# Kernel optimization log

Measured on AMD Instinct MI355X. Metric: run time of the kernel, lower is better.

Reference implementation:

```python
import jax, jax.numpy as jnp
import numpy as np

B, N, FEA = 64, 512, 102      # batch, motif points, feature cols (1 weight + 100 dist + 1 atom idx)
E = 10                         # expansion_size
d = 256                        # embed_dim
H = 4                          # num_heads
D = d * H                      # encoder working dim (embed_dim*num_heads)
L = 3                          # n_encoders
NATOM = 100                    # atom_init table rows
NDIST = FEA - 2                # 100 distance columns


def _ln(x, g, b, eps=1e-5):
    m = jnp.mean(x, -1, keepdims=True)
    v = jnp.mean((x - m) ** 2, -1, keepdims=True)
    return (x - m) / jnp.sqrt(v + eps) * g + b


def setup_inputs() -> dict:
    key = jax.random.key(0)
    ks = iter(jax.random.split(key, 40))

    def p(shape):
        return 0.02 * jax.random.normal(next(ks), shape, dtype=jnp.float32)

    # features: [:,:,0] = PDD weights (positive, row-normalized), [:,:,1:-1] = distances, [:,:,-1] = atom idx
    w = jax.random.uniform(next(ks), (B, N, 1), dtype=jnp.float32) + 1e-3
    w = w / jnp.sum(w, axis=1, keepdims=True)
    dist = jax.random.uniform(next(ks), (B, N, NDIST), dtype=jnp.float32)
    idx = jax.random.randint(next(ks), (B, N, 1), 0, NATOM).astype(jnp.float32)
    features = jnp.concatenate([w, dist, idx], axis=-1)

    inp = {
        "features": features,
        "atom_fea": p((NATOM, 92)),
        "comp_W": p((92, d)), "comp_b": p((d,)),
        "emb_W": p((NDIST * E, d)), "emb_b": p((d,)),
        "ln_g": jnp.ones((d,), jnp.float32), "ln_b": jnp.zeros((d,), jnp.float32),
        "enc_emb_W": p((L, d, D)), "enc_emb_b": p((L, D)),
        "enc_Wq_W": p((L, D, D)), "enc_Wq_b": p((L, D)),
        "enc_Wk_W": p((L, D, D)), "enc_Wk_b": p((L, D)),
        "enc_Wv_W": p((L, D, D)), "enc_Wv_b": p((L, D)),
        "enc_inq_W": p((L, D, D)), "enc_inq_b": p((L, D)),   # MHA in_proj (q part)
        "enc_ink_W": p((L, D, D)), "enc_ink_b": p((L, D)),   # MHA in_proj (k part)
        "enc_ln_g": jnp.ones((L, D), jnp.float32), "enc_ln_b": jnp.zeros((L, D), jnp.float32),
        "enc_out_W": p((L, D, d)), "enc_out_b": p((L, d)),
        "out_W": p((d, 1)), "out_b": p((1,)),
    }
    return inp


def reference(features, atom_fea, comp_W, comp_b, emb_W, emb_b, ln_g, ln_b,
              enc_emb_W, enc_emb_b, enc_Wq_W, enc_Wq_b, enc_Wk_W, enc_Wk_b,
              enc_Wv_W, enc_Wv_b, enc_inq_W, enc_inq_b, enc_ink_W, enc_ink_b,
              enc_ln_g, enc_ln_b, enc_out_W, enc_out_b, out_W, out_b):
    w = features[:, :, 0:1]                      # [B,N,1] PDD weights
    feat = features[:, :, 1:]
    idx = feat[:, :, -1].astype(jnp.int32)       # atom type index
    comp = atom_fea[idx] @ comp_W + comp_b       # [B,N,d]
    dist = feat[:, :, :-1]                       # [B,N,NDIST]
    starter = jnp.arange(E, dtype=features.dtype) / E
    de = (1.0 - (dist[..., None] - starter)) ** 2            # [B,N,NDIST,E]
    de = de.reshape(dist.shape[0], dist.shape[1], NDIST * E)
    strf = de @ emb_W + emb_b                    # [B,N,d]
    x = _ln(comp + strf, ln_g, ln_b)
    x_init = x
    dh = D // H
    scale = 1.0 / jnp.sqrt(jnp.asarray(dh, features.dtype))
    for l in range(L):
        e = x @ enc_emb_W[l] + enc_emb_b[l]                  # [B,N,D]
        mask = jnp.sum(jnp.abs(e), -1) == 0.0                # key padding mask [B,N]
        q = (e @ enc_Wq_W[l] + enc_Wq_b[l]) @ enc_inq_W[l] + enc_inq_b[l]
        k = (e @ enc_Wk_W[l] + enc_Wk_b[l]) @ enc_ink_W[l] + enc_ink_b[l]
        qh = q.reshape(q.shape[0], q.shape[1], H, dh)
        kh = k.reshape(k.shape[0], k.shape[1], H, dh)
        scores = jnp.einsum('bqhd,bkhd->bhqk', qh, kh) * scale
        scores = jnp.where(mask[:, None, None, :], -1e9, scores)
        A = jax.nn.softmax(scores, axis=-1).mean(axis=1)     # head-averaged attn weights [B,N,N]
        A = A * jnp.swapaxes(w, -2, -1)                      # external PDD reweighting
        A = A / jnp.sum(A, -1, keepdims=True)
        v = e @ enc_Wv_W[l] + enc_Wv_b[l]
        att = jnp.einsum('bij,bjd->bid', A, v)
        xe = _ln(e + jax.nn.softplus(att), enc_ln_g[l], enc_ln_b[l])
        x = xe @ enc_out_W[l] + enc_out_b[l]                 # back to [B,N,d]
    pooled = jnp.sum(w * (x + x_init), axis=1)               # weighted-sum pool [B,d]
    pooled = _ln(pooled, ln_g, ln_b)
    return pooled @ out_W + out_b                            # [B,1]
```

## Files before the change

kernel.cpp:

```cpp
#include <hip/hip_runtime.h>
#include <hip/hip_bf16.h>

#define PB 64
#define PN 512
#define PFEA 102
#define PE 10
#define PDD 256
#define PH 4
#define PDBIG 1024
#define PL 3
#define PNDIST 100

typedef __attribute__((ext_vector_type(8))) short s8b;
typedef __attribute__((ext_vector_type(4))) float f4;

typedef __attribute__((address_space(1))) const void gvoid_t;
typedef __attribute__((address_space(3))) void lvoid_t;
#define GLDS16(g, s) __builtin_amdgcn_global_load_lds((gvoid_t*)(g), (lvoid_t*)(s), 16, 0, 0)

union bfu { __hip_bfloat16 b; unsigned short u; };

__device__ __forceinline__ float b2f(unsigned short u) {
    return __uint_as_float((unsigned int)u << 16);
}
__device__ __forceinline__ unsigned short f2bu(float v) {
    bfu c; c.b = __float2bfloat16(v); return c.u;
}
__device__ __forceinline__ void split_bf16(float v, __hip_bfloat16& hi, __hip_bfloat16& lo) {
    hi = __float2bfloat16(v);
    lo = __float2bfloat16(v - __bfloat162float(hi));
}
__device__ __forceinline__ void split_u(float v, unsigned short& hu, unsigned short& lu) {
    __hip_bfloat16 h, l; split_bf16(v, h, l);
    bfu c; c.b = h; hu = c.u; c.b = l; lu = c.u;
}

__device__ __forceinline__ float block_sum1(float v, float* red, int tid) {
    #pragma unroll
    for (int off = 32; off >= 1; off >>= 1) v += __shfl_xor(v, off);
    __syncthreads();
    if ((tid & 63) == 0) red[tid >> 6] = v;
    __syncthreads();
    return red[0] + red[1] + red[2] + red[3];
}

template<int NR, bool MAXOP>
__device__ __forceinline__ void block_redN(float* v, float* red, int tid) {
    #pragma unroll
    for (int off = 32; off >= 1; off >>= 1) {
        #pragma unroll
        for (int r = 0; r < NR; ++r) {
            float o = __shfl_xor(v[r], off);
            v[r] = MAXOP ? fmaxf(v[r], o) : (v[r] + o);
        }
    }
    __syncthreads();
    if ((tid & 63) == 0) {
        #pragma unroll
        for (int r = 0; r < NR; ++r) red[(tid >> 6) * NR + r] = v[r];
    }
    __syncthreads();
    #pragma unroll
    for (int r = 0; r < NR; ++r) {
        float a = red[r], b = red[NR + r], c = red[2 * NR + r], d = red[3 * NR + r];
        v[r] = MAXOP ? fmaxf(fmaxf(a, b), fmaxf(c, d)) : ((a + b) + (c + d));
    }
    __syncthreads();
}

__global__ __launch_bounds__(256) void pst_atomproj(
    const float* __restrict__ atom_fea, const float* __restrict__ comp_W,
    float* __restrict__ atomP)
{
    int a = blockIdx.x, tid = threadIdx.x;
    __shared__ float af[92];
    if (tid < 92) af[tid] = atom_fea[a * 92 + tid];
    __syncthreads();
    float s = 0.0f;
    #pragma unroll 4
    for (int k = 0; k < 92; ++k) s = fmaf(af[k], comp_W[k * PDD + tid], s);
    atomP[a * PDD + tid] = s;
}

__global__ __launch_bounds__(256) void pst_embW_reduce(
    const float* __restrict__ emb_W, float* __restrict__ S0, float* __restrict__ S1)
{
    int f = blockIdx.x, tid = threadIdx.x;
    float s0 = 0.0f, s1 = 0.0f;
    #pragma unroll
    for (int t = 0; t < PE; ++t) {
        float w = emb_W[(f * PE + t) * PDD + tid];
        float tf = (float)t / (float)PE;
        s0 += w;
        s1 = fmaf(2.0f * tf, w, s1);
    }
    S0[f * PDD + tid] = s0;
    S1[f * PDD + tid] = s1;
}

__global__ __launch_bounds__(256) void pst_embW_const(
    const float* __restrict__ emb_W, const float* __restrict__ comp_b,
    const float* __restrict__ emb_b, float* __restrict__ Cv)
{
    int tid = threadIdx.x;
    float s = comp_b[tid] + emb_b[tid];
    for (int m = 0; m < PNDIST * PE; ++m) {
        float tf = (float)(m % PE) / (float)PE;
        s = fmaf(tf * tf, emb_W[m * PDD + tid], s);
    }
    Cv[tid] = s;
}

__global__ __launch_bounds__(256) void pst_wext(
    const float* __restrict__ features, float* __restrict__ wvec)
{
    long i = (long)blockIdx.x * 256 + threadIdx.x;
    wvec[i] = features[i * PFEA];
}

__global__ __launch_bounds__(256) void pst_embed16(
    const float* __restrict__ features, const float* __restrict__ atomP,
    const float* __restrict__ S0, const float* __restrict__ S1,
    const float* __restrict__ Cv, const float* __restrict__ ln_g,
    const float* __restrict__ ln_b, unsigned short* __restrict__ xpk)
{
    int r0 = blockIdx.x * 16, tid = threadIdx.x;
    __shared__ float uv[16][PNDIST];
    __shared__ int idxs[16];
    __shared__ float red[64];
    for (int m = tid; m < 16 * PNDIST; m += 256) {
        int r = m / PNDIST, f = m - r * PNDIST;
        uv[r][f] = 1.0f - features[(long)(r0 + r) * PFEA + 1 + f];
    }
    if (tid < 16) idxs[tid] = (int)features[(long)(r0 + tid) * PFEA + PFEA - 1];
    __syncthreads();

    float acc[16];
    float cv = Cv[tid];
    #pragma unroll
    for (int r = 0; r < 16; ++r) acc[r] = cv + atomP[idxs[r] * PDD + tid];
    for (int f = 0; f < PNDIST; f += 4) {
        float s0v[4], s1v[4];
        #pragma unroll
        for (int u = 0; u < 4; ++u) {
            s0v[u] = S0[(f + u) * PDD + tid];
            s1v[u] = S1[(f + u) * PDD + tid];
        }
        #pragma unroll
        for (int u = 0; u < 4; ++u) {
            #pragma unroll
            for (int r = 0; r < 16; ++r) {
                float uu = uv[r][f + u];
                acc[r] = fmaf(uu, fmaf(uu, s0v[u], s1v[u]), acc[r]);
            }
        }
    }
    float mean[16];
    #pragma unroll
    for (int r = 0; r < 16; ++r) mean[r] = acc[r];
    block_redN<16, false>(mean, red, tid);
    float var[16], dv[16];
    #pragma unroll
    for (int r = 0; r < 16; ++r) { mean[r] *= (1.0f / PDD); dv[r] = acc[r] - mean[r]; var[r] = dv[r] * dv[r]; }
    block_redN<16, false>(var, red, tid);
    #pragma unroll
    for (int r = 0; r < 16; ++r) {
        float y = dv[r] * rsqrtf(var[r] * (1.0f / PDD) + 1e-5f) * ln_g[tid] + ln_b[tid];
        long row = (long)(r0 + r);
        unsigned short hu, lu; split_u(y, hu, lu);
        xpk[row * 512 + tid] = hu;
        xpk[row * 512 + 256 + tid] = lu;
    }
}

template<int MODE, int VAR>
__global__ __launch_bounds__(256) void pst_gemm_bf16(
    const __hip_bfloat16* __restrict__ Ap, const __hip_bfloat16* __restrict__ Bp,
    const float* __restrict__ bias, float* __restrict__ C,
    __hip_bfloat16* __restrict__ P,
    int K, int Nw, long strideA, long strideB, long strideC)
{
    const int lda = (VAR == 1) ? K : 2 * K;
    const int ldb = (VAR == 1) ? K : 2 * K;
    int bz = blockIdx.z;
    Ap += (long)bz * strideA; Bp += (long)bz * strideB;
    if (MODE == 0) C += (long)bz * strideC;
    else P += (long)bz * strideC;

    int gx = gridDim.x, gy = gridDim.y;
    int lin = blockIdx.y * gx + blockIdx.x;
    int m0, n0;
    if (((gy & 3) == 0) && ((gx & 1) == 0)) {
        int rm = gy >> 2, rn = gx >> 1;
        int xcd = lin & 7, t = lin >> 3;
        int lm = t % rm, ln = t / rm;
        m0 = ((xcd >> 1) * rm + lm) * 128;
        n0 = ((xcd & 1) * rn + ln) * 128;
    } else {
        m0 = blockIdx.y * 128; n0 = blockIdx.x * 128;
    }

    __shared__ __hip_bfloat16 As[128 * 64];
    __shared__ __hip_bfloat16 Bs[128 * 64];

    int tid = threadIdx.x;
    int w = tid >> 6, l = tid & 63;
    int lr = l & 15, kb = l >> 4;
    int wm = (w >> 1) * 64, wn = (w & 1) * 64;
    int srow = tid >> 3;
    int sg = tid & 7;

    f4 acc[4][4] = {};

    const int K3 = (VAR == 0) ? 3 * K : ((VAR == 3) ? 2 * K : K);
    for (int k0 = 0; k0 < K3; k0 += 64) {
        int kA, kB;
        if (VAR == 0) { kA = (k0 < 2 * K) ? k0 : k0 - 2 * K; kB = (k0 < K) ? k0 : k0 - K; }
        else if (VAR == 3) { kA = k0; kB = (k0 < K) ? k0 : k0 - K; }
        else { kA = k0; kB = k0; }
        #pragma unroll
        for (int s = 0; s < 4; ++s) {
            int r = s * 32 + srow;
            int gsrc = sg ^ (r & 7);
            const __hip_bfloat16* ga = Ap + (long)(m0 + r) * lda + kA + gsrc * 8;
            const __hip_bfloat16* gb = Bp + (long)(n0 + r) * ldb + kB + gsrc * 8;
            GLDS16(ga, As + s * 2048 + w * 512);
            GLDS16(gb, Bs + s * 2048 + w * 512);
        }
        __syncthreads();

        #pragma unroll
        for (int kh = 0; kh < 2; ++kh) {
            s8b af[4], bf[4];
            #pragma unroll
            for (int f = 0; f < 4; ++f) {
                int ra = wm + f * 16 + lr;
                int rb = wn + f * 16 + lr;
                int gr = kh * 4 + kb;
                af[f] = *(const s8b*)(As + ra * 64 + ((gr ^ (ra & 7)) * 8));
                bf[f] = *(const s8b*)(Bs + rb * 64 + ((gr ^ (rb & 7)) * 8));
            }
            #pragma unroll
            for (int i = 0; i < 4; ++i)
                #pragma unroll
                for (int j = 0; j < 4; ++j)
                    acc[i][j] = __builtin_amdgcn_mfma_f32_16x16x32_bf16(af[i], bf[j], acc[i][j], 0, 0, 0);
        }
        __syncthreads();
    }

    #pragma unroll
    for (int i = 0; i < 4; ++i) {
        #pragma unroll
        for (int j = 0; j < 4; ++j) {
            int nbase = n0 + wn + j * 16 + lr;
            int mbase = m0 + wm + i * 16 + kb * 4;
            #pragma unroll
            for (int r = 0; r < 4; ++r) {
                int m = mbase + r;
                int n = nbase;
                float val = acc[i][j][r] + (bias ? bias[n] : 0.0f);
                if (MODE == 0) {
                    C[(long)m * Nw + n] = val;
                } else if (MODE == 4) {
                    __hip_bfloat16 hi, lo; split_bf16(val, hi, lo);
                    long b = (long)m * (2 * Nw) + n;
                    P[b] = hi; P[b + Nw] = lo;
                } else {
                    P[(long)m * Nw + n] = __float2bfloat16(val);
                }
            }
        }
    }
}

__global__ __launch_bounds__(512) void pst_gemm_qkv256(
    const __hip_bfloat16* __restrict__ Ap, const __hip_bfloat16* __restrict__ Bp,
    const float* __restrict__ bias,
    __hip_bfloat16* __restrict__ Pq, __hip_bfloat16* __restrict__ Pk,
    __hip_bfloat16* __restrict__ Pv, int K)
{
    extern __shared__ __hip_bfloat16 lds[];
    __hip_bfloat16* Asd = lds;
    __hip_bfloat16* Bsd = lds + 32768;

    const int lda = 2 * K;
    const int ldb = K;

    int gx = gridDim.x, gy = gridDim.y;
    int lin = blockIdx.y * gx + blockIdx.x;
    int m0, n0;
    if (((gy & 3) == 0) && ((gx & 1) == 0)) {
        int rm = gy >> 2, rn = gx >> 1;
        int xcd = lin & 7, t = lin >> 3;
        int lm = t % rm, ln = t / rm;
        m0 = ((xcd >> 1) * rm + lm) * 256;
        n0 = ((xcd & 1) * rn + ln) * 256;
    } else {
        m0 = blockIdx.y * 256; n0 = blockIdx.x * 256;
    }

    int tid = threadIdx.x;
    int w = tid >> 6, l = tid & 63;
    int lr = l & 15, kb = l >> 4;
    int wm = (w >> 2) * 128;
    int wn = (w & 3) * 64;
    int r6 = tid >> 3;
    int g  = tid & 7;

    f4 acc[8][4] = {};

    const int nt = K / 64;

    auto stage = [&](int tIdx, int buf) {
        int k0 = tIdx * 64;
        #pragma unroll
        for (int i = 0; i < 4; ++i) {
            int r = i * 64 + r6;
            int gs = g ^ (r & 7);
            GLDS16(Ap + (long)(m0 + r) * lda + k0 + gs * 8,
                   Asd + buf * 16384 + i * 4096 + w * 512);
            GLDS16(Bp + (long)(n0 + r) * ldb + k0 + gs * 8,
                   Bsd + buf * 16384 + i * 4096 + w * 512);
        }
    };

    stage(0, 0);
    __syncthreads();

    for (int t = 0; t < nt; ++t) {
        int cur = t & 1;
        if (t + 1 < nt) stage(t + 1, cur ^ 1);

        s8b bfr[4][2];
        #pragma unroll
        for (int fc = 0; fc < 4; ++fc) {
            int rb = wn + fc * 16 + lr;
            #pragma unroll
            for (int kh = 0; kh < 2; ++kh)
                bfr[fc][kh] = *(const s8b*)(Bsd + cur * 16384 + rb * 64 +
                                            (((kh * 4 + kb) ^ (rb & 7)) * 8));
        }
        #pragma unroll
        for (int q = 0; q < 4; ++q) {
            s8b afr[2][2];
            #pragma unroll
            for (int d = 0; d < 2; ++d) {
                int ra = wm + (q * 2 + d) * 16 + lr;
                #pragma unroll
                for (int kh = 0; kh < 2; ++kh)
                    afr[d][kh] = *(const s8b*)(Asd + cur * 16384 + ra * 64 +
                                               (((kh * 4 + kb) ^ (ra & 7)) * 8));
            }
            __builtin_amdgcn_s_setprio(1);
            #pragma unroll
            for (int d = 0; d < 2; ++d)
                #pragma unroll
                for (int fc = 0; fc < 4; ++fc)
                    #pragma unroll
                    for (int kh = 0; kh < 2; ++kh)
                        acc[q * 2 + d][fc] = __builtin_amdgcn_mfma_f32_16x16x32_bf16(
                            afr[d][kh], bfr[fc][kh], acc[q * 2 + d][fc], 0, 0, 0);
            __builtin_amdgcn_s_setprio(0);
        }
        __syncthreads();
    }

    #pragma unroll
    for (int i = 0; i < 8; ++i) {
        #pragma unroll
        for (int j = 0; j < 4; ++j) {
            int nbase = n0 + wn + j * 16 + lr;
            int mbase = m0 + wm + i * 16 + kb * 4;
            if ((nbase >> 10) == 2) {
                int np = nbase & 1023;
                unsigned short hu[4];
                #pragma unroll
                for (int r = 0; r < 4; ++r)
                    hu[r] = f2bu(acc[i][j][r] + bias[nbase]);
                int bb = mbase >> 9, rr0 = mbase & 511;
                unsigned short* pv = (unsigned short*)Pv + ((long)bb * PDBIG + np) * 512;
                *(ushort4*)(pv + rr0) = make_ushort4(hu[0], hu[1], hu[2], hu[3]);
            } else {
                #pragma unroll
                for (int r = 0; r < 4; ++r) {
                    int m = mbase + r;
                    int n = nbase;
                    float val = acc[i][j][r] + bias[n];
                    int bb = m >> 9, rr = m & 511;
                    int reg2 = n >> 10, np = n & 1023;
                    __hip_bfloat16* dst = (reg2 == 0) ? Pq : Pk;
                    int h = np >> 8, kk = np & 255;
                    dst[(((long)bb * 4 + h) * 512 + rr) * 256 + kk] = __float2bfloat16(val);
                }
            }
        }
    }
}

__global__ __launch_bounds__(256) void pst_pack_rows(
    const float* __restrict__ src, __hip_bfloat16* __restrict__ dst, int kshift)
{
    long i = (long)blockIdx.x * 256 + threadIdx.x;
    int K = 1 << kshift;
    long m = i >> kshift; int k = (int)(i & (K - 1));
    float v = src[i];
    __hip_bfloat16 hi, lo; split_bf16(v, hi, lo);
    long b = (m << (kshift + 1)) + k;
    dst[b] = hi; dst[b + K] = lo;
}

__global__ __launch_bounds__(256) void pst_packT_wL(
    const float* __restrict__ W, __hip_bfloat16* __restrict__ dst,
    int K, int N, long sSrc, long sDst)
{
    int lyr = blockIdx.y;
    long i = (long)blockIdx.x * 256 + threadIdx.x;
    int k = (int)(i / N), n = (int)(i - (long)k * N);
    float v = W[lyr * sSrc + i];
    __hip_bfloat16 hi, lo; split_bf16(v, hi, lo);
    long b = lyr * sDst + (long)n * (2 * K) + k;
    dst[b] = hi; dst[b + K] = lo;
}

__global__ __launch_bounds__(256) void pst_packT_single(
    const float* __restrict__ W, __hip_bfloat16* __restrict__ dst,
    int K, int N, long sSrc, long sDst)
{
    int lyr = blockIdx.y;
    long i = (long)blockIdx.x * 256 + threadIdx.x;
    int k = (int)(i / N), n = (int)(i - (long)k * N);
    float v = W[lyr * sSrc + i];
    dst[lyr * sDst + (long)n * K + k] = __float2bfloat16(v);
}

__global__ __launch_bounds__(256) void pst_bias_comb(
    const float* __restrict__ b1, const float* __restrict__ W2,
    const float* __restrict__ b2, float* __restrict__ out, int outOff)
{
    int lyr = blockIdx.y;
    int n = blockIdx.x * 256 + threadIdx.x;
    const float* b1l = b1 + (size_t)lyr * PDBIG;
    const float* W2l = W2 + (size_t)lyr * PDBIG * PDBIG;
    float s = b2[(size_t)lyr * PDBIG + n];
    for (int k2 = 0; k2 < PDBIG; ++k2)
        s = fmaf(b1l[k2], W2l[(long)k2 * PDBIG + n], s);
    out[(size_t)lyr * 3072 + outOff + n] = s;
}

__global__ __launch_bounds__(256) void pst_bias_oe(
    const float* __restrict__ bout, const float* __restrict__ Wemb,
    const float* __restrict__ bemb, float* __restrict__ boe)
{
    int lyr = blockIdx.y;
    int n = blockIdx.x * 256 + threadIdx.x;
    const float* b1 = bout + (size_t)lyr * PDD;
    const float* W  = Wemb + (size_t)(lyr + 1) * PDD * PDBIG;
    float s = bemb[(size_t)(lyr + 1) * PDBIG + n];
    #pragma unroll 4
    for (int k = 0; k < PDD; ++k)
        s = fmaf(b1[k], W[(long)k * PDBIG + n], s);
    boe[(size_t)lyr * PDBIG + n] = s;
}

__global__ __launch_bounds__(256) void pst_vbias(
    const float* __restrict__ src, float* __restrict__ out)
{
    int lyr = blockIdx.y;
    int i = blockIdx.x * 256 + threadIdx.x;
    out[(size_t)lyr * 3072 + 2048 + i] = src[(size_t)lyr * PDBIG + i];
}

__global__ __launch_bounds__(256) void pst_attnSM(
    const unsigned short* __restrict__ Sp, const float* __restrict__ wvec,
    __hip_bfloat16* __restrict__ Apack, int bGlobBase)
{
    int blk = blockIdx.x;
    int bLoc = blk >> 6;
    int q0 = (blk & 63) << 3;
    int tid = threadIdx.x;
    int w = tid >> 6, lane = tid & 63;
    int r0 = q0 + w * 2;
    int bGlob = bGlobBase + bLoc;

    float wcol[8];
    #pragma unroll
    for (int j = 0; j < 8; ++j)
        wcol[j] = wvec[(long)bGlob * PN + lane + 64 * j];
    const float scale = 0.0625f;
    float pacc[2][8] = {};

    for (int h = 0; h < PH; ++h) {
        const unsigned short* Sh = Sp + (((long)(bLoc * 4 + h)) * 512 + r0) * 512;
        #pragma unroll
        for (int rr = 0; rr < 2; ++rr) {
            float s[8]; float mx = -1e30f;
            #pragma unroll
            for (int j = 0; j < 8; ++j) {
                float a = b2f(Sh[(long)rr * 512 + lane + 64 * j]) * scale;
                s[j] = a; mx = fmaxf(mx, a);
            }
            #pragma unroll
            for (int off = 32; off >= 1; off >>= 1) mx = fmaxf(mx, __shfl_xor(mx, off));
            float sum = 0.0f;
            #pragma unroll
            for (int j = 0; j < 8; ++j) { s[j] = __expf(s[j] - mx); sum += s[j]; }
            #pragma unroll
            for (int off = 32; off >= 1; off >>= 1) sum += __shfl_xor(sum, off);
            float inv = 1.0f / sum;
            #pragma unroll
            for (int j = 0; j < 8; ++j) pacc[rr][j] = fmaf(s[j], inv, pacc[rr][j]);
        }
    }
    #pragma unroll
    for (int rr = 0; rr < 2; ++rr) {
        float asum = 0.0f;
        #pragma unroll
        for (int j = 0; j < 8; ++j) { pacc[rr][j] *= wcol[j]; asum += pacc[rr][j]; }
        #pragma unroll
        for (int off = 32; off >= 1; off >>= 1) asum += __shfl_xor(asum, off);
        float inv = 1.0f / asum;
        long rowb = ((long)bLoc * PN + r0 + rr) * 512;
        #pragma unroll
        for (int j = 0; j < 8; ++j) {
            int c = lane + 64 * j;
            Apack[rowb + c] = __float2bfloat16(pacc[rr][j] * inv);
        }
    }
}

__global__ __launch_bounds__(256) void pst_spln(
    const float* __restrict__ att, __hip_bfloat16* __restrict__ ep,
    const float* __restrict__ g, const float* __restrict__ bb)
{
    int r = blockIdx.x, tid = threadIdx.x;
    __shared__ float red[4];
    int i0 = tid * 4;
    unsigned short* epu = (unsigned short*)ep + (long)r * 2048;
    ushort4 h4 = *(const ushort4*)(epu + i0);
    ushort4 l4 = *(const ushort4*)(epu + 1024 + i0);
    float4 a4 = *(const float4*)(att + (long)r * 1024 + i0);
    float v[4];
    {
        float av[4] = {a4.x, a4.y, a4.z, a4.w};
        unsigned short hv[4] = {h4.x, h4.y, h4.z, h4.w};
        unsigned short lv[4] = {l4.x, l4.y, l4.z, l4.w};
        #pragma unroll
        for (int j = 0; j < 4; ++j) {
            float a = av[j];
            float sp = (a > 20.0f) ? a : log1pf(expf(a));
            v[j] = b2f(hv[j]) + b2f(lv[j]) + sp;
        }
    }
    float s = v[0] + v[1] + v[2] + v[3];
    float mean = block_sum1(s, red, tid) * (1.0f / PDBIG);
    float vs = 0.0f;
    #pragma unroll
    for (int j = 0; j < 4; ++j) { float dv = v[j] - mean; vs += dv * dv; }
    float var = block_sum1(vs, red, tid) * (1.0f / PDBIG);
    float inv = rsqrtf(var + 1e-5f);
    float4 g4 = *(const float4*)(g + i0);
    float4 b4 = *(const float4*)(bb + i0);
    float gv[4] = {g4.x, g4.y, g4.z, g4.w};
    float bv[4] = {b4.x, b4.y, b4.z, b4.w};
    unsigned short ho[4], lo_[4];
    #pragma unroll
    for (int j = 0; j < 4; ++j) {
        float y = (v[j] - mean) * inv * gv[j] + bv[j];
        split_u(y, ho[j], lo_[j]);
    }
    *(ushort4*)(epu + i0)        = make_ushort4(ho[0], ho[1], ho[2], ho[3]);
    *(ushort4*)(epu + 1024 + i0) = make_ushort4(lo_[0], lo_[1], lo_[2], lo_[3]);
}

__global__ __launch_bounds__(256) void pst_pool1(
    const float* __restrict__ wvec, const unsigned short* __restrict__ pk,
    float* __restrict__ partial)
{
    int p = blockIdx.x, b = blockIdx.y, tid = threadIdx.x;
    float acc = 0.0f;
    for (int n = p * 64; n < p * 64 + 64; ++n) {
        float w = wvec[(long)b * PN + n];
        long row = (long)b * PN + n;
        float xv = b2f(pk[row * 512 + tid]) + b2f(pk[row * 512 + 256 + tid]);
        acc = fmaf(w, xv, acc);
    }
    partial[((long)b * 8 + p) * PDD + tid] = acc;
}

__global__ __launch_bounds__(256) void pst_pool2(
    const float* __restrict__ partial, const float* __restrict__ partiali,
    const float* __restrict__ ln_g, const float* __restrict__ ln_b,
    const float* __restrict__ out_W, const float* __restrict__ out_b,
    float* __restrict__ out)
{
    int b = blockIdx.x, tid = threadIdx.x;
    __shared__ float red[4];
    float acc = 0.0f;
    #pragma unroll
    for (int p = 0; p < 8; ++p)
        acc += partial[((long)b * 8 + p) * PDD + tid] + partiali[((long)b * 8 + p) * PDD + tid];
    float mean = block_sum1(acc, red, tid) * (1.0f / PDD);
    float dv = acc - mean;
    float var = block_sum1(dv * dv, red, tid) * (1.0f / PDD);
    float y = dv * rsqrtf(var + 1e-5f) * ln_g[tid] + ln_b[tid];
    float s = block_sum1(y * out_W[tid], red, tid);
    if (tid == 0) out[b] = s + out_b[0];
}

template<int MODE, int VAR>
static void launch_gbf(const __hip_bfloat16* A, const __hip_bfloat16* B, const float* bias,
                       float* C, __hip_bfloat16* P, int M, int Nw, int K,
                       long sA, long sB, long sC, int batch, hipStream_t st)
{
    dim3 grid(Nw / 128, M / 128, batch);
    pst_gemm_bf16<MODE, VAR><<<grid, dim3(256), 0, st>>>(A, B, bias, C, P, K, Nw, sA, sB, sC);
}

extern "C" void kernel_launch(void* const* d_in, const int* in_sizes, int n_in,
                              void* d_out, int out_size, void* d_ws, size_t ws_size,
                              hipStream_t stream)
{
    const float* features  = (const float*)d_in[0];
    const float* atom_fea  = (const float*)d_in[1];
    const float* comp_W    = (const float*)d_in[2];
    const float* comp_b    = (const float*)d_in[3];
    const float* emb_W     = (const float*)d_in[4];
    const float* emb_b     = (const float*)d_in[5];
    const float* ln_g      = (const float*)d_in[6];
    const float* ln_b      = (const float*)d_in[7];
    const float* enc_emb_W = (const float*)d_in[8];
    const float* enc_emb_b = (const float*)d_in[9];
    const float* enc_Wq_W  = (const float*)d_in[10];
    const float* enc_Wq_b  = (const float*)d_in[11];
    const float* enc_Wk_W  = (const float*)d_in[12];
    const float* enc_Wk_b  = (const float*)d_in[13];
    const float* enc_Wv_W  = (const float*)d_in[14];
    const float* enc_Wv_b  = (const float*)d_in[15];
    const float* enc_inq_W = (const float*)d_in[16];
    const float* enc_inq_b = (const float*)d_in[17];
    const float* enc_ink_W = (const float*)d_in[18];
    const float* enc_ink_b = (const float*)d_in[19];
    const float* enc_ln_g  = (const float*)d_in[20];
    const float* enc_ln_b  = (const float*)d_in[21];
    const float* enc_out_W = (const float*)d_in[22];
    const float* enc_out_b = (const float*)d_in[23];
    const float* out_W     = (const float*)d_in[24];
    const float* out_b     = (const float*)d_in[25];

    float* ws = (float*)d_ws;
    size_t off = 0;
    unsigned short* xpk  = (unsigned short*)(ws + off); off += (size_t)PB * PN * 512 / 2;
    __hip_bfloat16* WembT = (__hip_bfloat16*)(ws + off); off += (size_t)PL * 1024 * 512 / 2;
    __hip_bfloat16* WqkvT = (__hip_bfloat16*)(ws + off); off += (size_t)PL * 3072 * 1024 / 2;
    __hip_bfloat16* WoutT2 = (__hip_bfloat16*)(ws + off); off += (size_t)256 * 2048 / 2;
    __hip_bfloat16* WoeT  = (__hip_bfloat16*)(ws + off); off += (size_t)2 * 1024 * 2048 / 2;
    float* bqkv  = ws + off; off += (size_t)PL * 3072;
    float* boe   = ws + off; off += (size_t)2 * PDBIG;
    float* atomP = ws + off; off += (size_t)100 * PDD;
    float* S0v   = ws + off; off += (size_t)PNDIST * PDD;
    float* S1v   = ws + off; off += (size_t)PNDIST * PDD;
    float* Cv    = ws + off; off += PDD;
    float* partial  = ws + off; off += (size_t)PB * 8 * PDD;
    float* partiali = ws + off; off += (size_t)PB * 8 * PDD;
    float* wvec  = ws + off; off += (size_t)PB * PN;
    size_t persistf = off;

    const size_t PRE_FL = (size_t)3 * 1024 * 2048 / 2 * 2 + (size_t)3 * 1024 * 1024;
    const size_t ROW_FL = 4608;
    int CB = 64;
    while (CB > 1) {
        size_t M = (size_t)CB * PN;
        size_t region = M * ROW_FL;
        if (region < PRE_FL) region = PRE_FL;
        if ((persistf + region) * sizeof(float) <= ws_size) break;
        CB >>= 1;
    }
    const size_t M = (size_t)CB * PN;

    float* base = ws + persistf;
    __hip_bfloat16* pA = (__hip_bfloat16*)base;
    __hip_bfloat16* pB = (__hip_bfloat16*)(base + 3145728);
    float* Wtmp3 = base + 6291456;
    __hip_bfloat16* B0    = (__hip_bfloat16*)(base);
    __hip_bfloat16* B1    = (__hip_bfloat16*)(base + M * 1024);
    __hip_bfloat16* qp    = (__hip_bfloat16*)(base + M * 2048);
    __hip_bfloat16* kp    = (__hip_bfloat16*)(base + M * 2560);
    __hip_bfloat16* vpT   = (__hip_bfloat16*)(base + M * 3072);
    unsigned short* Spack = (unsigned short*)(base + M * 3584);
    float* attb           = base + M * 3584;

    pst_atomproj<<<dim3(100), 256, 0, stream>>>(atom_fea, comp_W, atomP);
    pst_embW_reduce<<<dim3(PNDIST), 256, 0, stream>>>(emb_W, S0v, S1v);
    pst_embW_const<<<dim3(1), 256, 0, stream>>>(emb_W, comp_b, emb_b, Cv);
    pst_wext<<<dim3(PB * PN / 256), 256, 0, stream>>>(features, wvec);

    const long WS = 1024L * 1024;
    const long WE = 256L * 1024;
    const long SQK = 3072L * 1024;
    pst_packT_wL<<<dim3(WE / 256, 3), 256, 0, stream>>>(enc_emb_W, WembT, 256, 1024, WE, 1024L * 512);
    pst_pack_rows<<<dim3(3 * WS / 256), 256, 0, stream>>>(enc_Wq_W, pA, 10);
    pst_packT_wL<<<dim3(WS / 256, 3), 256, 0, stream>>>(enc_inq_W, pB, 1024, 1024, WS, 1024L * 2048);
    launch_gbf<0, 0>(pA, pB, nullptr, Wtmp3, nullptr,
                     1024, 1024, 1024, 1024L * 2048, 1024L * 2048, WS, 3, stream);
    pst_packT_single<<<dim3(WS / 256, 3), 256, 0, stream>>>(Wtmp3, WqkvT, 1024, 1024, WS, SQK);
    pst_bias_comb<<<dim3(4, 3), 256, 0, stream>>>(enc_Wq_b, enc_inq_W, enc_inq_b, bqkv, 0);
    pst_pack_rows<<<dim3(3 * WS / 256), 256, 0, stream>>>(enc_Wk_W, pA, 10);
    pst_packT_wL<<<dim3(WS / 256, 3), 256, 0, stream>>>(enc_ink_W, pB, 1024, 1024, WS, 1024L * 2048);
    launch_gbf<0, 0>(pA, pB, nullptr, Wtmp3, nullptr,
                     1024, 1024, 1024, 1024L * 2048, 1024L * 2048, WS, 3, stream);
    pst_packT_single<<<dim3(WS / 256, 3), 256, 0, stream>>>(Wtmp3, WqkvT + 1024L * 1024, 1024, 1024, WS, SQK);
    pst_bias_comb<<<dim3(4, 3), 256, 0, stream>>>(enc_Wk_b, enc_ink_W, enc_ink_b, bqkv, 1024);
    pst_packT_single<<<dim3(WS / 256, 3), 256, 0, stream>>>(enc_Wv_W, WqkvT + 2048L * 1024, 1024, 1024, WS, SQK);
    pst_vbias<<<dim3(4, 3), 256, 0, stream>>>(enc_Wv_b, bqkv);
    pst_packT_wL<<<dim3(WE / 256, 1), 256, 0, stream>>>(enc_out_W + 2 * WE, WoutT2, 1024, 256, WE, 256L * 2048);
    pst_pack_rows<<<dim3(2 * WE / 256), 256, 0, stream>>>(enc_out_W, pA, 8);
    launch_gbf<0, 0>(pA, WembT + 1024L * 512, nullptr, Wtmp3, nullptr,
                     1024, 1024, 256, 1024L * 512, 1024L * 512, WS, 2, stream);
    pst_packT_wL<<<dim3(WS / 256, 2), 256, 0, stream>>>(Wtmp3, WoeT, 1024, 1024, WS, 1024L * 2048);
    pst_bias_oe<<<dim3(4, 2), 256, 0, stream>>>(enc_out_b, enc_emb_W, enc_emb_b, boe);

    pst_embed16<<<dim3(PB * PN / 16), 256, 0, stream>>>(
        features, atomP, S0v, S1v, Cv, ln_g, ln_b, xpk);
    pst_pool1<<<dim3(8, PB), 256, 0, stream>>>(wvec, xpk, partiali);

    hipFuncSetAttribute((const void*)pst_gemm_qkv256,
                        hipFuncAttributeMaxDynamicSharedMemorySize, 131072);

    for (int cb0 = 0; cb0 < PB; cb0 += CB) {
        const int Mi = (int)M;
        __hip_bfloat16* xps = (__hip_bfloat16*)xpk + (size_t)cb0 * PN * 512;
        __hip_bfloat16* eP = B0;
        __hip_bfloat16* qP2 = B1;
        launch_gbf<4, 3>(xps, WembT, enc_emb_b, nullptr, eP,
                         Mi, PDBIG, PDD, 0, 0, 0, 1, stream);
        for (int l = 0; l < PL; ++l) {
            __hip_bfloat16* Apack = qp;
            {
                dim3 grid(3072 / 256, Mi / 256, 1);
                pst_gemm_qkv256<<<grid, dim3(512), 131072, stream>>>(
                    eP, WqkvT + (size_t)l * SQK, bqkv + (size_t)l * 3072,
                    qp, kp, vpT, PDBIG);
            }
            launch_gbf<5, 1>(qp, kp, nullptr, nullptr, (__hip_bfloat16*)Spack,
                             512, 512, 256, 512L * 256, 512L * 256, 512L * 512,
                             CB * 4, stream);
            pst_attnSM<<<dim3(CB * 64), 256, 0, stream>>>(Spack, wvec, Apack, cb0);
            launch_gbf<0, 1>(Apack, vpT, nullptr, attb, nullptr,
                             512, PDBIG, 512, 512L * 512, 1024L * 512, 512L * 1024,
                             CB, stream);
            pst_spln<<<dim3(Mi), 256, 0, stream>>>(
                attb, eP, enc_ln_g + (size_t)l * PDBIG, enc_ln_b + (size_t)l * PDBIG);
            if (l < PL - 1) {
                launch_gbf<4, 3>(eP, WoeT + (size_t)l * 1024 * 2048, boe + (size_t)l * PDBIG,
                                 nullptr, qP2, Mi, PDBIG, PDBIG, 0, 0, 0, 1, stream);
                __hip_bfloat16* t = eP; eP = qP2; qP2 = t;
            } else {
                launch_gbf<4, 3>(eP, WoutT2, enc_out_b + 2 * (size_t)PDD,
                                 nullptr, xps, Mi, PDD, PDBIG, 0, 0, 0, 1, stream);
            }
        }
    }

    pst_pool1<<<dim3(8, PB), 256, 0, stream>>>(wvec, xpk, partial);
    pst_pool2<<<dim3(PB), 256, 0, stream>>>(partial, partiali, ln_g, ln_b, out_W, out_b,
                                            (float*)d_out);
}
```

Before: 3.224 ms.

## Lower precision of weight-combine GEMMs and attention output, parallelize bias combine

The Wq·inq and Wk·ink weight-product precomputes drop the hi/lo split-bf16 packing and use single bf16 operands, halving the K dimension of those GEMMs. The attention-times-V output is written as bf16 instead of fp32, and the softplus/LayerNorm kernel reads bf16. The bias-combine kernel splits its 1024-long reduction across four wavefronts with a shared-memory sum and launches more blocks. This reduces memory traffic and precompute cost but lowers numerical accuracy of the fused weights and the attention output.

```diff
diff --git a/kernel.cpp b/kernel.cpp
--- a/kernel.cpp
+++ b/kernel.cpp
@@ -410,6 +410,13 @@
     dst[b] = hi; dst[b + K] = lo;
 }
 
+__global__ __launch_bounds__(256) void pst_pack_single(
+    const float* __restrict__ src, __hip_bfloat16* __restrict__ dst)
+{
+    long i = (long)blockIdx.x * 256 + threadIdx.x;
+    dst[i] = __float2bfloat16(src[i]);
+}
+
 __global__ __launch_bounds__(256) void pst_packT_wL(
     const float* __restrict__ W, __hip_bfloat16* __restrict__ dst,
     int K, int N, long sSrc, long sDst)
@@ -439,13 +446,24 @@
     const float* __restrict__ b2, float* __restrict__ out, int outOff)
 {
     int lyr = blockIdx.y;
-    int n = blockIdx.x * 256 + threadIdx.x;
+    int tid = threadIdx.x;
+    int nl = tid & 63;
+    int kq = tid >> 6;
+    int n = blockIdx.x * 64 + nl;
     const float* b1l = b1 + (size_t)lyr * PDBIG;
     const float* W2l = W2 + (size_t)lyr * PDBIG * PDBIG;
-    float s = b2[(size_t)lyr * PDBIG + n];
-    for (int k2 = 0; k2 < PDBIG; ++k2)
+    __shared__ float part[4][64];
+    float s = 0.0f;
+    for (int k2 = kq * 256; k2 < kq * 256 + 256; ++k2)
         s = fmaf(b1l[k2], W2l[(long)k2 * PDBIG + n], s);
-    out[(size_t)lyr * 3072 + outOff + n] = s;
+    part[kq][nl] = s;
+    __syncthreads();
+    if (tid < 64) {
+        int nn = blockIdx.x * 64 + tid;
+        out[(size_t)lyr * 3072 + outOff + nn] =
+            ((part[0][tid] + part[1][tid]) + (part[2][tid] + part[3][tid]))
+            + b2[(size_t)lyr * PDBIG + nn];
+    }
 }
 
 __global__ __launch_bounds__(256) void pst_bias_oe(
@@ -530,7 +548,7 @@
 }
 
 __global__ __launch_bounds__(256) void pst_spln(
-    const float* __restrict__ att, __hip_bfloat16* __restrict__ ep,
+    const unsigned short* __restrict__ att, __hip_bfloat16* __restrict__ ep,
     const float* __restrict__ g, const float* __restrict__ bb)
 {
     int r = blockIdx.x, tid = threadIdx.x;
@@ -539,15 +557,15 @@
     unsigned short* epu = (unsigned short*)ep + (long)r * 2048;
     ushort4 h4 = *(const ushort4*)(epu + i0);
     ushort4 l4 = *(const ushort4*)(epu + 1024 + i0);
-    float4 a4 = *(const float4*)(att + (long)r * 1024 + i0);
+    ushort4 a4 = *(const ushort4*)(att + (long)r * 1024 + i0);
     float v[4];
     {
-        float av[4] = {a4.x, a4.y, a4.z, a4.w};
+        unsigned short av[4] = {a4.x, a4.y, a4.z, a4.w};
         unsigned short hv[4] = {h4.x, h4.y, h4.z, h4.w};
         unsigned short lv[4] = {l4.x, l4.y, l4.z, l4.w};
         #pragma unroll
         for (int j = 0; j < 4; ++j) {
-            float a = av[j];
+            float a = b2f(av[j]);
             float sp = (a > 20.0f) ? a : log1pf(expf(a));
             v[j] = b2f(hv[j]) + b2f(lv[j]) + sp;
         }
@@ -666,7 +684,7 @@
     float* wvec  = ws + off; off += (size_t)PB * PN;
     size_t persistf = off;
 
-    const size_t PRE_FL = (size_t)3 * 1024 * 2048 / 2 * 2 + (size_t)3 * 1024 * 1024;
+    const size_t PRE_FL = (size_t)3 * 1024 * 1024 / 2 * 2 + (size_t)3 * 1024 * 1024;
     const size_t ROW_FL = 4608;
     int CB = 64;
     while (CB > 1) {
@@ -680,15 +698,16 @@
 
     float* base = ws + persistf;
     __hip_bfloat16* pA = (__hip_bfloat16*)base;
-    __hip_bfloat16* pB = (__hip_bfloat16*)(base + 3145728);
-    float* Wtmp3 = base + 6291456;
+    __hip_bfloat16* pB = (__hip_bfloat16*)(base + 1572864);
+    float* Wtmp3 = base + 3145728;
     __hip_bfloat16* B0    = (__hip_bfloat16*)(base);
     __hip_bfloat16* B1    = (__hip_bfloat16*)(base + M * 1024);
     __hip_bfloat16* qp    = (__hip_bfloat16*)(base + M * 2048);
     __hip_bfloat16* kp    = (__hip_bfloat16*)(base + M * 2560);
     __hip_bfloat16* vpT   = (__hip_bfloat16*)(base + M * 3072);
     unsigned short* Spack = (unsigned short*)(base + M * 3584);
-    float* attb           = base + M * 3584;
+    unsigned short* attb  = (unsigned short*)(base + M * 3584);
+
 
     pst_atomproj<<<dim3(100), 256, 0, stream>>>(atom_fea, comp_W, atomP);
     pst_embW_reduce<<<dim3(PNDIST), 256, 0, stream>>>(emb_W, S0v, S1v);
@@ -699,23 +718,23 @@
     const long WE = 256L * 1024;
     const long SQK = 3072L * 1024;
     pst_packT_wL<<<dim3(WE / 256, 3), 256, 0, stream>>>(enc_emb_W, WembT, 256, 1024, WE, 1024L * 512);
-    pst_pack_rows<<<dim3(3 * WS / 256), 256, 0, stream>>>(enc_Wq_W, pA, 10);
-    pst_packT_wL<<<dim3(WS / 256, 3), 256, 0, stream>>>(enc_inq_W, pB, 1024, 1024, WS, 1024L * 2048);
-    launch_gbf<0, 0>(pA, pB, nullptr, Wtmp3, nullptr,
-                     1024, 1024, 1024, 1024L * 2048, 1024L * 2048, WS, 3, stream);
+    pst_pack_single<<<dim3(3 * WS / 256), 256, 0, stream>>>(enc_Wq_W, pA);
+    pst_packT_single<<<dim3(WS / 256, 3), 256, 0, stream>>>(enc_inq_W, pB, 1024, 1024, WS, WS);
+    launch_gbf<0, 1>(pA, pB, nullptr, Wtmp3, nullptr,
+                     1024, 1024, 1024, WS, WS, WS, 3, stream);
     pst_packT_single<<<dim3(WS / 256, 3), 256, 0, stream>>>(Wtmp3, WqkvT, 1024, 1024, WS, SQK);
-    pst_bias_comb<<<dim3(4, 3), 256, 0, stream>>>(enc_Wq_b, enc_inq_W, enc_inq_b, bqkv, 0);
-    pst_pack_rows<<<dim3(3 * WS / 256), 256, 0, stream>>>(enc_Wk_W, pA, 10);
-    pst_packT_wL<<<dim3(WS / 256, 3), 256, 0, stream>>>(enc_ink_W, pB, 1024, 1024, WS, 1024L * 2048);
-    launch_gbf<0, 0>(pA, pB, nullptr, Wtmp3, nullptr,
-                     1024, 1024, 1024, 1024L * 2048, 1024L * 2048, WS, 3, stream);
+    pst_bias_comb<<<dim3(16, 3), 256, 0, stream>>>(enc_Wq_b, enc_inq_W, enc_inq_b, bqkv, 0);
+    pst_pack_single<<<dim3(3 * WS / 256), 256, 0, stream>>>(enc_Wk_W, pA);
+    pst_packT_single<<<dim3(WS / 256, 3), 256, 0, stream>>>(enc_ink_W, pB, 1024, 1024, WS, WS);
+    launch_gbf<0, 1>(pA, pB, nullptr, Wtmp3, nullptr,
+                     1024, 1024, 1024, WS, WS, WS, 3, stream);
     pst_packT_single<<<dim3(WS / 256, 3), 256, 0, stream>>>(Wtmp3, WqkvT + 1024L * 1024, 1024, 1024, WS, SQK);
-    pst_bias_comb<<<dim3(4, 3), 256, 0, stream>>>(enc_Wk_b, enc_ink_W, enc_ink_b, bqkv, 1024);
+    pst_bias_comb<<<dim3(16, 3), 256, 0, stream>>>(enc_Wk_b, enc_ink_W, enc_ink_b, bqkv, 1024);
     pst_packT_single<<<dim3(WS / 256, 3), 256, 0, stream>>>(enc_Wv_W, WqkvT + 2048L * 1024, 1024, 1024, WS, SQK);
     pst_vbias<<<dim3(4, 3), 256, 0, stream>>>(enc_Wv_b, bqkv);
     pst_packT_wL<<<dim3(WE / 256, 1), 256, 0, stream>>>(enc_out_W + 2 * WE, WoutT2, 1024, 256, WE, 256L * 2048);
     pst_pack_rows<<<dim3(2 * WE / 256), 256, 0, stream>>>(enc_out_W, pA, 8);
-    launch_gbf<0, 0>(pA, WembT + 1024L * 512, nullptr, Wtmp3, nullptr,
+    launch_gbf<0, 3>(pA, WembT + 1024L * 512, nullptr, Wtmp3, nullptr,
                      1024, 1024, 256, 1024L * 512, 1024L * 512, WS, 2, stream);
     pst_packT_wL<<<dim3(WS / 256, 2), 256, 0, stream>>>(Wtmp3, WoeT, 1024, 1024, WS, 1024L * 2048);
     pst_bias_oe<<<dim3(4, 2), 256, 0, stream>>>(enc_out_b, enc_emb_W, enc_emb_b, boe);
@@ -746,7 +765,7 @@
                              512, 512, 256, 512L * 256, 512L * 256, 512L * 512,
                              CB * 4, stream);
             pst_attnSM<<<dim3(CB * 64), 256, 0, stream>>>(Spack, wvec, Apack, cb0);
-            launch_gbf<0, 1>(Apack, vpT, nullptr, attb, nullptr,
+            launch_gbf<5, 1>(Apack, vpT, nullptr, nullptr, (__hip_bfloat16*)attb,
                              512, PDBIG, 512, 512L * 512, 1024L * 512, 512L * 1024,
                              CB, stream);
             pst_spln<<<dim3(Mi), 256, 0, stream>>>(
```

Result: faster. 3.033 ms (-5.9%).
